# Optimization experiments

Hardware: AMD Instinct MI355X
Metric: run time of the kernel (lower is better)

Reference implementation:

```python
import jax, jax.numpy as jnp
import numpy as np

D = 512
H = 8
DK = D // H
EXP = 2
EPS = 1e-5


def _layernorm(x, g, b):
    mu = jnp.mean(x, axis=-1, keepdims=True)
    var = jnp.mean(jnp.square(x - mu), axis=-1, keepdims=True)
    return (x - mu) * jax.lax.rsqrt(var + EPS) * g + b


def setup_inputs() -> dict:
    key = jax.random.key(0)
    ks = jax.random.split(key, 10)
    B, C = 4, 2048
    s = 0.02
    return {
        "h": jax.random.normal(ks[0], (B, C, D), jnp.float32),
        "adj_bias": jax.random.normal(ks[1], (B, C, C), jnp.float32),
        "w_qkv": jax.random.normal(ks[2], (D, 3 * D), jnp.float32) * s,
        "b_qkv": jnp.zeros((3 * D,), jnp.float32),
        "w_out": jax.random.normal(ks[3], (D, D), jnp.float32) * s,
        "b_out": jnp.zeros((D,), jnp.float32),
        "ln1_g": jnp.ones((D,), jnp.float32),
        "ln1_b": jnp.zeros((D,), jnp.float32),
        "ln2_g": jnp.ones((D,), jnp.float32),
        "ln2_b": jnp.zeros((D,), jnp.float32),
        "w1": jax.random.normal(ks[4], (D, D * EXP), jnp.float32) * s,
        "b1": jnp.zeros((D * EXP,), jnp.float32),
        "w2": jax.random.normal(ks[5], (D * EXP, D), jnp.float32) * s,
        "b2": jnp.zeros((D,), jnp.float32),
    }


def reference(h, adj_bias, w_qkv, b_qkv, w_out, b_out, ln1_g, ln1_b, ln2_g, ln2_b, w1, b1, w2, b2):
    B, C, _ = h.shape
    scale = DK ** -0.5
    h_n = _layernorm(h, ln1_g, ln1_b)
    qkv = (h_n @ w_qkv + b_qkv).reshape(B, C, 3, H, DK)
    q, k, v = (qkv[:, :, i].transpose(0, 2, 1, 3) for i in range(3))  # (B,H,C,DK)
    logits = jnp.einsum('bhqd,bhkd->bhqk', q, k) * scale + adj_bias[:, None, :, :]
    attn = jax.nn.softmax(logits, axis=-1)  # (B,H,C,C); dropout off (eval)
    out = jnp.einsum('bhqk,bhkd->bhqd', attn, v).transpose(0, 2, 1, 3).reshape(B, C, D)
    h = h + out @ w_out + b_out
    ff = _layernorm(h, ln2_g, ln2_b)
    ff = jax.nn.gelu(ff @ w1 + b1, approximate=False) @ w2 + b2
    return h + ff
```

## Files before the change

### kernel.cpp

```cpp
#include <hip/hip_runtime.h>
#include <hip/hip_bf16.h>

#define BDIM 4
#define CDIM 2048
#define DDIM 512
#define HH   8
#define DKH  64
#define NROW (BDIM * CDIM)

typedef unsigned short u16;
typedef unsigned int   u32;
typedef u16   u16x4  __attribute__((ext_vector_type(4)));
typedef u16   u16x8  __attribute__((ext_vector_type(8)));
typedef u32   u32x4  __attribute__((ext_vector_type(4)));
typedef __bf16 bf16x8 __attribute__((ext_vector_type(8)));
typedef __bf16 bf16x2 __attribute__((ext_vector_type(2)));
typedef float f32x4  __attribute__((ext_vector_type(4)));
typedef float f32x16 __attribute__((ext_vector_type(16)));

#define LOG2E 1.4426950408889634f

__device__ __forceinline__ u16 f2bf(float f) {
  union { float f; unsigned u; } x; x.f = f;
  unsigned u = x.u;
  u += 0x7fffu + ((u >> 16) & 1u);
  return (u16)(u >> 16);
}
__device__ __forceinline__ float bf2f(u16 u) {
  return __builtin_bit_cast(float, (u32)u << 16);
}
__device__ __forceinline__ u32 pk2(float a, float b) {
  bf16x2 t; t[0] = (__bf16)a; t[1] = (__bf16)b;
  return __builtin_bit_cast(u32, t);
}
__device__ __forceinline__ float fexp2(float x) {
  float r;
  asm("v_exp_f32 %0, %1" : "=v"(r) : "v"(x));
  return r;
}

__device__ __forceinline__ void gload_lds16(const u16* gp, u16* lp) {
  __builtin_amdgcn_global_load_lds((__attribute__((address_space(1))) const void*)gp,
                                   (__attribute__((address_space(3))) void*)lp, 16, 0, 0);
}

__device__ __forceinline__ void ln_body(int bx, int tid,
                                        const float* __restrict__ x,
                                        const float* __restrict__ gamma,
                                        const float* __restrict__ beta,
                                        u16* __restrict__ y) {
  int gw = (bx * 256 + tid) >> 6;
  int l  = tid & 63;
  const float* xr = x + (size_t)gw * DDIM;
  float4 a = *(const float4*)(xr + l * 8);
  float4 b = *(const float4*)(xr + l * 8 + 4);
  float s = a.x + a.y + a.z + a.w + b.x + b.y + b.z + b.w;
  float q = a.x*a.x + a.y*a.y + a.z*a.z + a.w*a.w + b.x*b.x + b.y*b.y + b.z*b.z + b.w*b.w;
#pragma unroll
  for (int m = 1; m < 64; m <<= 1) { s += __shfl_xor(s, m); q += __shfl_xor(q, m); }
  float mu  = s * (1.0f / DDIM);
  float var = q * (1.0f / DDIM) - mu * mu;
  float rs  = rsqrtf(var + 1e-5f);
  float4 g0 = *(const float4*)(gamma + l * 8);
  float4 g1 = *(const float4*)(gamma + l * 8 + 4);
  float4 b0 = *(const float4*)(beta + l * 8);
  float4 b1 = *(const float4*)(beta + l * 8 + 4);
  u16x8 o;
  o[0] = f2bf((a.x - mu) * rs * g0.x + b0.x);
  o[1] = f2bf((a.y - mu) * rs * g0.y + b0.y);
  o[2] = f2bf((a.z - mu) * rs * g0.z + b0.z);
  o[3] = f2bf((a.w - mu) * rs * g0.w + b0.w);
  o[4] = f2bf((b.x - mu) * rs * g1.x + b1.x);
  o[5] = f2bf((b.y - mu) * rs * g1.y + b1.y);
  o[6] = f2bf((b.z - mu) * rs * g1.z + b1.z);
  o[7] = f2bf((b.w - mu) * rs * g1.w + b1.w);
  *(u16x8*)(y + (size_t)gw * DDIM + l * 8) = o;
}

__global__ __launch_bounds__(256) void ln_kernel(const float* __restrict__ x,
                                                 const float* __restrict__ gamma,
                                                 const float* __restrict__ beta,
                                                 u16* __restrict__ y) {
  ln_body(blockIdx.x, threadIdx.x, x, gamma, beta, y);
}

__device__ __forceinline__ void adj_body(int f, int t,
                                         const float* __restrict__ adj,
                                         u16* __restrict__ adjC) {
  const int b = f >> 8, kt = (f >> 3) & 31;
  const int q0 = (f & 7) * 256;
  const int ch = t & 7, c16 = ch & 3, hi2 = ch >> 2, m = c16 >> 1;
  const int K0 = m * 32 + ((c16 * 2) & 3) * 8 + hi2 * 4;
#pragma unroll
  for (int itq = 0; itq < 8; ++itq) {
    int q = q0 + itq * 32 + (t >> 3);
    const float* src = adj + ((size_t)b * CDIM + q) * CDIM + kt * 64;
    f32x4 v0 = *(const f32x4*)(src + K0);
    f32x4 v1 = *(const f32x4*)(src + K0 + 8);
    u16x8 o;
    o[0] = f2bf(v0[0] * LOG2E); o[1] = f2bf(v0[1] * LOG2E);
    o[2] = f2bf(v0[2] * LOG2E); o[3] = f2bf(v0[3] * LOG2E);
    o[4] = f2bf(v1[0] * LOG2E); o[5] = f2bf(v1[1] * LOG2E);
    o[6] = f2bf(v1[2] * LOG2E); o[7] = f2bf(v1[3] * LOG2E);
    *(u16x8*)(adjC + ((size_t)(b * 32 + kt) * 2048 + q) * 64 + ch * 8) = o;
  }
}

__global__ __launch_bounds__(256) void setup_kernel(const float* __restrict__ h,
                                                    const float* __restrict__ ln1g,
                                                    const float* __restrict__ ln1b,
                                                    u16* __restrict__ hn,
                                                    const float* __restrict__ wqkv,
                                                    const float* __restrict__ wout,
                                                    const float* __restrict__ w1,
                                                    const float* __restrict__ w2,
                                                    u16* __restrict__ o_qkv,
                                                    u16* __restrict__ o_out,
                                                    u16* __restrict__ o_w1,
                                                    u16* __restrict__ o_w2) {
  const int bx = blockIdx.x;
  const int t = threadIdx.x;
  if (bx < 2048) {
    ln_body(bx, t, h, ln1g, ln1b, hn);
  } else {
    int idx = (bx - 2048) * 256 + t;
    const float* w; u16* wt; int K, N;
    if (idx < 98304)       { w = wqkv; wt = o_qkv; K = 512;  N = 1536; }
    else if (idx < 131072) { idx -= 98304;  w = wout; wt = o_out; K = 512;  N = 512; }
    else if (idx < 196608) { idx -= 131072; w = w1;   wt = o_w1;  K = 512;  N = 1024; }
    else                   { idx -= 196608; w = w2;   wt = o_w2;  K = 1024; N = 512; }
    int kb = K >> 3;
    int n = idx / kb, k0 = (idx - n * kb) * 8;
    u16x8 o;
#pragma unroll
    for (int j = 0; j < 8; ++j) o[j] = f2bf(w[(size_t)(k0 + j) * N + n]);
    *(u16x8*)(wt + (size_t)n * K + k0) = o;
  }
}

template <int EPI>
__device__ __forceinline__ void gemm_epi(int row, int col, float val, int N,
                                         const float* __restrict__ res,
                                         float* __restrict__ outf,
                                         u16* __restrict__ outb,
                                         u16* __restrict__ outq,
                                         u16* __restrict__ outk,
                                         u16* __restrict__ outv) {
  if constexpr (EPI == 0) {
    int t = col >> 9, hh = (col >> 6) & 7, dk = col & 63;
    int bb = row >> 11, cc = row & 2047;
    if (t == 0) {
      val *= 0.125f * LOG2E;
      outq[(((size_t)bb * HH + hh) * CDIM + cc) * DKH + dk] = f2bf(val);
    } else if (t == 1) {
      outk[(((size_t)bb * HH + hh) * CDIM + cc) * DKH + dk] = f2bf(val);
    } else {
      outv[(((size_t)bb * HH + hh) * DKH + dk) * CDIM + cc] = f2bf(val);
    }
  } else if constexpr (EPI == 1) {
    size_t idx = (size_t)row * N + col;
    outf[idx] = val + res[idx];
  } else {
    float g = 0.5f * val * (1.0f + erff(val * 0.70710678118f));
    outb[(size_t)row * N + col] = f2bf(g);
  }
}

template <int EPI>
__device__ __forceinline__ void gemm128_body(int flat, int nbn, int nwg,
                                             const u16* __restrict__ A,
                                             const u16* __restrict__ Bt,
                                             const float* __restrict__ bias,
                                             const float* __restrict__ res,
                                             float* __restrict__ outf,
                                             u16* __restrict__ outb,
                                             u16* __restrict__ outq,
                                             u16* __restrict__ outk,
                                             u16* __restrict__ outv,
                                             int N, int K) {
  __shared__ u16 As[2][128 * 64];
  __shared__ u16 Bs[2][128 * 64];
  const int tid = threadIdx.x;
  const int w = tid >> 6, l = tid & 63;
  const int l15 = l & 15, l4 = l >> 4, l7 = l15 & 7;
  const int virt = (flat & 7) * (nwg >> 3) + (flat >> 3);
  const int bn = virt % nbn, bm = virt / nbn;
  const int wr = w >> 1, wc = w & 1;

  f32x4 acc[4][4] = {};

  const int sg = (l & 7) ^ (l >> 3);
  const u16* Ag = A  + (size_t)(bm * 128 + w * 32 + (l >> 3)) * K + sg * 8;
  const u16* Bg = Bt + (size_t)(bn * 128 + w * 32 + (l >> 3)) * K + sg * 8;

  auto stage = [&](int buf, int k0) {
#pragma unroll
    for (int i = 0; i < 4; ++i) {
      gload_lds16(Ag + (size_t)(8 * i) * K + k0, &As[buf][(w * 32 + 8 * i) * 64]);
      gload_lds16(Bg + (size_t)(8 * i) * K + k0, &Bs[buf][(w * 32 + 8 * i) * 64]);
    }
  };

  stage(0, 0);
  __syncthreads();
  int cur = 0;
  for (int k0 = 0; k0 < K; k0 += 64) {
    if (k0 + 64 < K) stage(cur ^ 1, k0 + 64);
#pragma unroll
    for (int s = 0; s < 2; ++s) {
      bf16x8 af[4], bf[4];
#pragma unroll
      for (int m = 0; m < 4; ++m)
        af[m] = *(const bf16x8*)(&As[cur][(wr * 64 + m * 16 + l15) * 64 + (((s * 4 + l4) ^ l7) * 8)]);
#pragma unroll
      for (int n = 0; n < 4; ++n)
        bf[n] = *(const bf16x8*)(&Bs[cur][(wc * 64 + n * 16 + l15) * 64 + (((s * 4 + l4) ^ l7) * 8)]);
#pragma unroll
      for (int m = 0; m < 4; ++m)
#pragma unroll
        for (int n = 0; n < 4; ++n)
          acc[m][n] = __builtin_amdgcn_mfma_f32_16x16x32_bf16(af[m], bf[n], acc[m][n], 0, 0, 0);
    }
    __syncthreads();
    cur ^= 1;
  }

#pragma unroll
  for (int m = 0; m < 4; ++m) {
    const int row0 = bm * 128 + wr * 64 + m * 16 + l4 * 4;
#pragma unroll
    for (int n = 0; n < 4; ++n) {
      const int col = bn * 128 + wc * 64 + n * 16 + l15;
      const float bv = bias[col];
#pragma unroll
      for (int r = 0; r < 4; ++r)
        gemm_epi<EPI>(row0 + r, col, acc[m][n][r] + bv, N, res, outf, outb, outq, outk, outv);
    }
  }
}

__global__ __launch_bounds__(256) void qkv_adj_kernel(const u16* __restrict__ A,
                                                      const u16* __restrict__ Bt,
                                                      const float* __restrict__ bias,
                                                      u16* __restrict__ outq,
                                                      u16* __restrict__ outk,
                                                      u16* __restrict__ outv,
                                                      const float* __restrict__ adj,
                                                      u16* __restrict__ adjC) {
  if (blockIdx.x < 768) {
    gemm128_body<0>(blockIdx.x, 12, 768, A, Bt, bias, nullptr,
                    nullptr, nullptr, outq, outk, outv, 3 * DDIM, DDIM);
  } else {
    adj_body(blockIdx.x - 768, threadIdx.x, adj, adjC);
  }
}

template <int EPI>
__global__ __launch_bounds__(256) void gemm128k(const u16* __restrict__ A,
                                                const u16* __restrict__ Bt,
                                                const float* __restrict__ bias,
                                                const float* __restrict__ res,
                                                float* __restrict__ outf,
                                                u16* __restrict__ outb,
                                                int M, int N, int K) {
  gemm128_body<EPI>(blockIdx.x + gridDim.x * blockIdx.y, gridDim.x,
                    gridDim.x * gridDim.y, A, Bt, bias, res,
                    outf, outb, nullptr, nullptr, nullptr, N, K);
}

template <int EPI>
__global__ __launch_bounds__(256) void gemm64(const u16* __restrict__ A,
                                              const u16* __restrict__ Bt,
                                              const float* __restrict__ bias,
                                              const float* __restrict__ res,
                                              float* __restrict__ outf,
                                              u16* __restrict__ outb,
                                              int M, int N, int K) {
  __shared__ u16 As[2][64 * 64];
  __shared__ u16 Bs[2][128 * 64];
  const int tid = threadIdx.x;
  const int w = tid >> 6, l = tid & 63;
  const int l15 = l & 15, l4 = l >> 4, l7 = l15 & 7;
  const int nbn = gridDim.x, nwg = gridDim.x * gridDim.y;
  const int flat = blockIdx.x + nbn * blockIdx.y;
  const int virt = (flat & 7) * (nwg >> 3) + (flat >> 3);
  const int bn = virt % nbn, bm = virt / nbn;

  f32x4 acc[4][2] = {};

  const int sg = (l & 7) ^ (l >> 3);
  const u16* Ag = A  + (size_t)(bm * 64  + w * 16 + (l >> 3)) * K + sg * 8;
  const u16* Bg = Bt + (size_t)(bn * 128 + w * 32 + (l >> 3)) * K + sg * 8;

  auto stage = [&](int buf, int k0) {
    gload_lds16(Ag + k0,                  &As[buf][(w * 16 + 0) * 64]);
    gload_lds16(Ag + (size_t)8 * K + k0,  &As[buf][(w * 16 + 8) * 64]);
    gload_lds16(Bg + k0,                  &Bs[buf][(w * 32 + 0) * 64]);
    gload_lds16(Bg + (size_t)8 * K + k0,  &Bs[buf][(w * 32 + 8) * 64]);
    gload_lds16(Bg + (size_t)16 * K + k0, &Bs[buf][(w * 32 + 16) * 64]);
    gload_lds16(Bg + (size_t)24 * K + k0, &Bs[buf][(w * 32 + 24) * 64]);
  };

  stage(0, 0);
  __syncthreads();
  int cur = 0;
  for (int k0 = 0; k0 < K; k0 += 64) {
    if (k0 + 64 < K) stage(cur ^ 1, k0 + 64);
#pragma unroll
    for (int s = 0; s < 2; ++s) {
      bf16x8 af[4], bf[2];
#pragma unroll
      for (int m = 0; m < 4; ++m)
        af[m] = *(const bf16x8*)(&As[cur][(m * 16 + l15) * 64 + (((s * 4 + l4) ^ l7) * 8)]);
#pragma unroll
      for (int n = 0; n < 2; ++n)
        bf[n] = *(const bf16x8*)(&Bs[cur][(w * 32 + n * 16 + l15) * 64 + (((s * 4 + l4) ^ l7) * 8)]);
#pragma unroll
      for (int m = 0; m < 4; ++m)
#pragma unroll
        for (int n = 0; n < 2; ++n)
          acc[m][n] = __builtin_amdgcn_mfma_f32_16x16x32_bf16(af[m], bf[n], acc[m][n], 0, 0, 0);
    }
    __syncthreads();
    cur ^= 1;
  }

#pragma unroll
  for (int m = 0; m < 4; ++m) {
    const int row0 = bm * 64 + m * 16 + l4 * 4;
#pragma unroll
    for (int n = 0; n < 2; ++n) {
      const int col = bn * 128 + w * 32 + n * 16 + l15;
      const float bv = bias[col];
#pragma unroll
      for (int r = 0; r < 4; ++r)
        gemm_epi<EPI>(row0 + r, col, acc[m][n][r] + bv, N, res, outf, outb,
                      nullptr, nullptr, nullptr);
    }
  }
}

__global__ __launch_bounds__(512, 2) void flash_attn(const u16* __restrict__ Q,
                                                     const u16* __restrict__ Kg,
                                                     const u16* __restrict__ Vt,
                                                     const u16* __restrict__ adjC,
                                                     u16* __restrict__ O) {
  __shared__ u16 Ks[2][2][64 * 64];
  __shared__ u16 Vs[2][2][64 * 64];
  __shared__ float lw[4][32];
  __shared__ float lsx[4][32];
  const int flat = blockIdx.x + 16 * blockIdx.y;
  const int virt = (flat & 7) * 64 + (flat >> 3);
  const int qt = virt & 15;
  const int bh = virt >> 4;
  const int b = bh >> 3, hh = bh & 7;
  const int tid = threadIdx.x;
  const int w = tid >> 6, l = tid & 63;
  const int kh = w >> 2, qg = w & 3;
  const int q32 = l & 31, hi = l >> 5;
  const int qglob = qt * 128 + qg * 32 + q32;

  const u16* Qb = Q  + (size_t)bh * CDIM * DKH;
  const u16* Kb = Kg + (size_t)bh * CDIM * DKH;
  const u16* Vb = Vt + (size_t)bh * DKH * CDIM;

  const int srow = qg * 16 + (l >> 3);
  const int sg   = (l & 7) ^ (l >> 3);
  const u16* Kg0 = Kb + (size_t)(srow + 0) * DKH + sg * 8;
  const u16* Kg1 = Kb + (size_t)(srow + 8) * DKH + sg * 8;
  const u16* Vg0 = Vb + (size_t)(srow + 0) * CDIM + sg * 8;
  const u16* Vg1 = Vb + (size_t)(srow + 8) * CDIM + sg * 8;

  bf16x8 qf[4];
#pragma unroll
  for (int s = 0; s < 4; ++s)
    qf[s] = *(const bf16x8*)(Qb + (size_t)qglob * DKH + s * 16 + hi * 8);

  const u16* adjQ = adjC + ((size_t)(b * 32) * 2048 + qglob) * 64 + hi * 32;

  f32x16 oa[2] = {};
  float lsum = 0.f;

  auto stage = [&](int buf, int ktr) {
    int kta = kh * 16 + ktr;
    gload_lds16(Kg0 + (size_t)kta * 4096, &Ks[kh][buf][(qg * 16 + 0) * 64]);
    gload_lds16(Kg1 + (size_t)kta * 4096, &Ks[kh][buf][(qg * 16 + 8) * 64]);
    gload_lds16(Vg0 + kta * 64, &Vs[kh][buf][(qg * 16 + 0) * 64]);
    gload_lds16(Vg1 + kta * 64, &Vs[kh][buf][(qg * 16 + 8) * 64]);
  };
  auto ajload = [&](u16x8* dst, int ktr) {
    const u16* p = adjQ + (size_t)(kh * 16 + ktr) * 131072;
#pragma unroll
    for (int i = 0; i < 4; ++i) dst[i] = *(const u16x8*)(p + i * 8);
  };
  auto computeQK = [&](const u16* KsB, const u16x8* av, f32x16* sa) {
#pragma unroll
    for (int m = 0; m < 2; ++m)
#pragma unroll
      for (int r = 0; r < 16; ++r)
        sa[m][r] = bf2f(av[m * 2 + (r >> 3)][r & 7]);
    __builtin_amdgcn_s_setprio(1);
#pragma unroll
    for (int s = 0; s < 4; ++s)
#pragma unroll
      for (int m = 0; m < 2; ++m) {
        bf16x8 kf = *(const bf16x8*)(&KsB[(m * 32 + q32) * 64 + (((s * 2 + hi) ^ (q32 & 7)) * 8)]);
        sa[m] = __builtin_amdgcn_mfma_f32_32x32x16_bf16(kf, qf[s], sa[m], 0, 0, 0);
      }
    __builtin_amdgcn_s_setprio(0);
  };
  auto computePV = [&](const u16* VsB, f32x16* sa) {
#pragma unroll
    for (int m = 0; m < 2; ++m)
#pragma unroll
      for (int r = 0; r < 16; ++r) {
        float p = fexp2(sa[m][r]);
        sa[m][r] = p;
        lsum += p;
      }
    bf16x8 af[4];
#pragma unroll
    for (int m = 0; m < 2; ++m)
#pragma unroll
      for (int t2 = 0; t2 < 2; ++t2) {
        u32 w0 = pk2(sa[m][t2 * 8 + 0], sa[m][t2 * 8 + 1]);
        u32 w1 = pk2(sa[m][t2 * 8 + 2], sa[m][t2 * 8 + 3]);
        u32 w2 = pk2(sa[m][t2 * 8 + 4], sa[m][t2 * 8 + 5]);
        u32 w3 = pk2(sa[m][t2 * 8 + 6], sa[m][t2 * 8 + 7]);
        auto r02 = __builtin_amdgcn_permlane32_swap(w0, w2, false, false);
        auto r13 = __builtin_amdgcn_permlane32_swap(w1, w3, false, false);
        u32x4 aw;
        aw[0] = r02[0];
        aw[1] = r13[0];
        aw[2] = r02[1];
        aw[3] = r13[1];
        af[m * 2 + t2] = __builtin_bit_cast(bf16x8, aw);
      }
    __builtin_amdgcn_s_setprio(1);
#pragma unroll
    for (int s = 0; s < 4; ++s)
#pragma unroll
      for (int n = 0; n < 2; ++n) {
        bf16x8 vf = *(const bf16x8*)(&VsB[(n * 32 + q32) * 64 + (((s * 2 + hi) ^ (q32 & 7)) * 8)]);
        oa[n] = __builtin_amdgcn_mfma_f32_32x32x16_bf16(af[s], vf, oa[n], 0, 0, 0);
      }
    __builtin_amdgcn_s_setprio(0);
  };

  u16x8 avA[4], avB[4];
  f32x16 sa[2];
  stage(0, 0);
  ajload(avA, 0);
  __syncthreads();
#pragma unroll 1
  for (int it = 0; it < 8; ++it) {
    int ktr = it * 2;
    stage(1, ktr + 1);
    computeQK(&Ks[kh][0][0], avA, sa);
    ajload(avB, ktr + 1);
    computePV(&Vs[kh][0][0], sa);
    __syncthreads();
    if (ktr + 2 < 16) stage(0, ktr + 2);
    computeQK(&Ks[kh][1][0], avB, sa);
    if (ktr + 2 < 16) ajload(avA, ktr + 2);
    computePV(&Vs[kh][1][0], sa);
    __syncthreads();
  }

  lsum += __shfl_xor(lsum, 32);

  float* cb = (float*)&Vs[0][0][0];
  if (kh == 1) {
#pragma unroll
    for (int n = 0; n < 2; ++n)
#pragma unroll
      for (int r = 0; r < 16; ++r)
        cb[((qg * 2 + n) * 16 + r) * 64 + l] = oa[n][r];
    if (hi == 0) lsx[qg][q32] = lsum;
  }
  __syncthreads();
  if (kh == 0) {
    lsum += lsx[qg][q32];
#pragma unroll
    for (int n = 0; n < 2; ++n)
#pragma unroll
      for (int r = 0; r < 16; ++r)
        oa[n][r] += cb[((qg * 2 + n) * 16 + r) * 64 + l];
    lw[qg][q32] = 1.0f / lsum;
#pragma unroll
    for (int n = 0; n < 2; ++n)
#pragma unroll
      for (int r = 0; r < 16; ++r) {
        int qloc = (r & 3) + 8 * (r >> 2) + 4 * hi;
        int row = qt * 128 + qg * 32 + qloc;
        float val = oa[n][r] * lw[qg][qloc];
        O[((size_t)b * CDIM + row) * DDIM + hh * 64 + n * 32 + q32] = f2bf(val);
      }
  }
}

extern "C" void kernel_launch(void* const* d_in, const int* in_sizes, int n_in,
                              void* d_out, int out_size, void* d_ws, size_t ws_size,
                              hipStream_t stream) {
  const float* h      = (const float*)d_in[0];
  const float* adj    = (const float*)d_in[1];
  const float* w_qkv  = (const float*)d_in[2];
  const float* b_qkv  = (const float*)d_in[3];
  const float* w_out  = (const float*)d_in[4];
  const float* b_out  = (const float*)d_in[5];
  const float* ln1g   = (const float*)d_in[6];
  const float* ln1b   = (const float*)d_in[7];
  const float* ln2g   = (const float*)d_in[8];
  const float* ln2b   = (const float*)d_in[9];
  const float* w1     = (const float*)d_in[10];
  const float* b1     = (const float*)d_in[11];
  const float* w2     = (const float*)d_in[12];
  const float* b2     = (const float*)d_in[13];
  float* out = (float*)d_out;

  char* ws = (char*)d_ws;
  u16* adjC  = (u16*)(ws);
  u16* hn    = (u16*)(ws + 33554432);
  u16* qb    = (u16*)(ws + 41943040);
  u16* kb    = (u16*)(ws + 50331648);
  u16* vt    = (u16*)(ws + 58720256);
  u16* attn  = (u16*)(ws + 67108864);
  u16* wqkvt = (u16*)(ws + 75497472);
  u16* woutt = (u16*)(ws + 77070336);
  u16* w1t   = (u16*)(ws + 77594624);
  u16* w2t   = (u16*)(ws + 78643200);
  u16* ffin  = hn;
  u16* ffmid = qb;

  setup_kernel<<<3072, 256, 0, stream>>>(h, ln1g, ln1b, hn,
                                         w_qkv, w_out, w1, w2,
                                         wqkvt, woutt, w1t, w2t);

  qkv_adj_kernel<<<1792, 256, 0, stream>>>(hn, wqkvt, b_qkv, qb, kb, vt,
                                           adj, adjC);

  flash_attn<<<dim3(16, 32), 512, 0, stream>>>(qb, kb, vt, adjC, attn);

  gemm64<1><<<dim3(4, 128), 256, 0, stream>>>(attn, woutt, b_out, h,
                                              out, nullptr, NROW, DDIM, DDIM);

  ln_kernel<<<2048, 256, 0, stream>>>(out, ln2g, ln2b, ffin);

  gemm128k<2><<<dim3(8, 64), 256, 0, stream>>>(ffin, w1t, b1, nullptr,
                                               nullptr, ffmid, NROW, 2 * DDIM, DDIM);

  gemm64<1><<<dim3(4, 128), 256, 0, stream>>>(ffmid, w2t, b2, out,
                                              out, nullptr, NROW, DDIM, 2 * DDIM);
}
```

Measured before the change: 181.8 us.

## Use triple-buffered K=32 LDS stages with one barrier per step in GEMM

The shared GEMM body switches from a double-buffered K=64 tile to a triple-buffered K=32 tile. It uses explicit vmcnt waits and a single raw s_barrier per iteration in place of two __syncthreads. The swizzle is changed to fit 32-element rows. The aim is to cut barrier overhead and let the next tile's loads overlap the current MFMAs. In exchange, each barrier covers half as many MFMAs, and the ring buffer's correctness depends on the three-stage reuse distance.

```diff
diff --git a/kernel.cpp b/kernel.cpp
--- a/kernel.cpp
+++ b/kernel.cpp
@@ -19,6 +19,12 @@
 typedef float f32x16 __attribute__((ext_vector_type(16)));
 
 #define LOG2E 1.4426950408889634f
+
+#define MEMFENCE asm volatile("" ::: "memory")
+__device__ __forceinline__ void sbar() {
+  MEMFENCE; __builtin_amdgcn_s_barrier(); MEMFENCE;
+}
+#define VMWAIT(N) asm volatile("s_waitcnt vmcnt(" #N ")" ::: "memory")
 
 __device__ __forceinline__ u16 f2bf(float f) {
   union { float f; unsigned u; } x; x.f = f;
@@ -178,51 +184,56 @@
                                              u16* __restrict__ outk,
                                              u16* __restrict__ outv,
                                              int N, int K) {
-  __shared__ u16 As[2][128 * 64];
-  __shared__ u16 Bs[2][128 * 64];
+  __shared__ u16 As[3][128 * 32];
+  __shared__ u16 Bs[3][128 * 32];
   const int tid = threadIdx.x;
   const int w = tid >> 6, l = tid & 63;
-  const int l15 = l & 15, l4 = l >> 4, l7 = l15 & 7;
+  const int l15 = l & 15, l4 = l >> 4;
   const int virt = (flat & 7) * (nwg >> 3) + (flat >> 3);
   const int bn = virt % nbn, bm = virt / nbn;
   const int wr = w >> 1, wc = w & 1;
 
   f32x4 acc[4][4] = {};
 
-  const int sg = (l & 7) ^ (l >> 3);
-  const u16* Ag = A  + (size_t)(bm * 128 + w * 32 + (l >> 3)) * K + sg * 8;
-  const u16* Bg = Bt + (size_t)(bn * 128 + w * 32 + (l >> 3)) * K + sg * 8;
+  const int sg = (l & 3) ^ ((l >> 2) & 3);
+  const u16* Ag = A  + (size_t)(bm * 128 + w * 32 + (l >> 2)) * K + sg * 8;
+  const u16* Bg = Bt + (size_t)(bn * 128 + w * 32 + (l >> 2)) * K + sg * 8;
 
   auto stage = [&](int buf, int k0) {
-#pragma unroll
-    for (int i = 0; i < 4; ++i) {
-      gload_lds16(Ag + (size_t)(8 * i) * K + k0, &As[buf][(w * 32 + 8 * i) * 64]);
-      gload_lds16(Bg + (size_t)(8 * i) * K + k0, &Bs[buf][(w * 32 + 8 * i) * 64]);
+    gload_lds16(Ag + k0,                  &As[buf][(w * 32 + 0) * 32]);
+    gload_lds16(Ag + (size_t)16 * K + k0, &As[buf][(w * 32 + 16) * 32]);
+    gload_lds16(Bg + k0,                  &Bs[buf][(w * 32 + 0) * 32]);
+    gload_lds16(Bg + (size_t)16 * K + k0, &Bs[buf][(w * 32 + 16) * 32]);
+  };
+
+  const int nk = K >> 5;
+  stage(0, 0);
+  int bcur = 0, bnxt = 1;
+#pragma unroll 1
+  for (int i = 0; i < nk; ++i) {
+    if (i + 1 < nk) {
+      stage(bnxt, (i + 1) * 32);
+      VMWAIT(4);
+    } else {
+      VMWAIT(0);
     }
-  };
-
-  stage(0, 0);
-  __syncthreads();
-  int cur = 0;
-  for (int k0 = 0; k0 < K; k0 += 64) {
-    if (k0 + 64 < K) stage(cur ^ 1, k0 + 64);
-#pragma unroll
-    for (int s = 0; s < 2; ++s) {
-      bf16x8 af[4], bf[4];
-#pragma unroll
-      for (int m = 0; m < 4; ++m)
-        af[m] = *(const bf16x8*)(&As[cur][(wr * 64 + m * 16 + l15) * 64 + (((s * 4 + l4) ^ l7) * 8)]);
+    sbar();
+    const u16* AsC = &As[bcur][0];
+    const u16* BsC = &Bs[bcur][0];
+    bf16x8 af[4], bf[4];
+#pragma unroll
+    for (int m = 0; m < 4; ++m)
+      af[m] = *(const bf16x8*)(&AsC[(wr * 64 + m * 16 + l15) * 32 + ((l4 ^ (l15 & 3)) * 8)]);
+#pragma unroll
+    for (int n = 0; n < 4; ++n)
+      bf[n] = *(const bf16x8*)(&BsC[(wc * 64 + n * 16 + l15) * 32 + ((l4 ^ (l15 & 3)) * 8)]);
+#pragma unroll
+    for (int m = 0; m < 4; ++m)
 #pragma unroll
       for (int n = 0; n < 4; ++n)
-        bf[n] = *(const bf16x8*)(&Bs[cur][(wc * 64 + n * 16 + l15) * 64 + (((s * 4 + l4) ^ l7) * 8)]);
-#pragma unroll
-      for (int m = 0; m < 4; ++m)
-#pragma unroll
-        for (int n = 0; n < 4; ++n)
-          acc[m][n] = __builtin_amdgcn_mfma_f32_16x16x32_bf16(af[m], bf[n], acc[m][n], 0, 0, 0);
-    }
-    __syncthreads();
-    cur ^= 1;
+        acc[m][n] = __builtin_amdgcn_mfma_f32_16x16x32_bf16(af[m], bf[n], acc[m][n], 0, 0, 0);
+    bcur = bnxt;
+    bnxt = bnxt + 1 == 3 ? 0 : bnxt + 1;
   }
 
 #pragma unroll
```

After: 176.7 us. -2.8%, faster.
